# Performance work log

Hardware: AMD Instinct MI355X
Metric: run time of the kernel (lower is better)

## Reference

```python
import jax, jax.numpy as jnp
import numpy as np

ALPHA = 0.2  # leakyrelu negative slope and residual scale


def setup_inputs() -> dict:
    key = jax.random.key(0)
    k1, k2, k3, k4 = jax.random.split(key, 4)
    B, N, C, F = 8, 2048, 128, 128
    text = jax.random.normal(k1, (B, N, C), dtype=jnp.float32)
    adj = jax.random.uniform(k2, (B, N, N), dtype=jnp.float32)  # unused by the layer's math
    W = jax.random.normal(k3, (C, F), dtype=jnp.float32) * (1.0 / np.sqrt(C))
    a = jax.random.normal(k4, (2 * F, 1), dtype=jnp.float32) * 0.1
    return {"text": text, "adj": adj, "W": W, "a": a}


def reference(text, adj, W, a):
    # h: [B, N, F]
    h = jnp.matmul(text, W)
    Fdim = W.shape[1]
    a1 = a[:Fdim, 0]  # applies to source node i
    a2 = a[Fdim:, 0]  # applies to target node j
    e1 = jnp.einsum('bnf,f->bn', h, a1)  # [B, N]
    e2 = jnp.einsum('bnf,f->bn', h, a2)  # [B, N]
    # scores[b,i,j] = leakyrelu(a1.h_i + a2.h_j)  (same as concat-matmul in original)
    scores = jax.nn.leaky_relu(e1[:, :, None] + e2[:, None, :], negative_slope=ALPHA)
    attention = jax.nn.softmax(scores, axis=2)  # [B, N, N]; dropout off (eval)
    h_prime = jnp.matmul(attention, h)  # [B, N, F]
    return jax.nn.elu(h_prime + ALPHA * h)
```

## Files before the change

kernel.cpp:

```cpp
#include <hip/hip_runtime.h>
#include <hip/hip_bf16.h>

#define BB 8
#define NN 2048
#define CC 128
#define FF 128
#define ALPHA 0.2f
#define ROWS 16
#define WTPAD 136
#define CHN 256
#define CLEN 8
#define CSH 3

typedef __hip_bfloat16 bf16;
typedef __attribute__((ext_vector_type(8))) short short8;
typedef __attribute__((ext_vector_type(4))) float f32x4;

__device__ __forceinline__ float ld1(const void* p, int i, int f32) {
    if (f32) return ((const float*)p)[i];
    return __bfloat162float(((const bf16*)p)[i]);
}
__device__ __forceinline__ float2 ld2(const void* p, int pair, int f32) {
    if (f32) return ((const float2*)p)[pair];
    __hip_bfloat162 v = ((const __hip_bfloat162*)p)[pair];
    return make_float2(__bfloat162float(v.x), __bfloat162float(v.y));
}

__global__ __launch_bounds__(256) void k_prep(const void* __restrict__ text,
                                              const void* __restrict__ W,
                                              const void* __restrict__ a,
                                              int* __restrict__ flag,
                                              float* __restrict__ wa1,
                                              float* __restrict__ wa2,
                                              ushort* __restrict__ WT) {
    __shared__ int cnt;
    __shared__ float aL[2 * FF];
    const int t = threadIdx.x;
    if (t == 0) cnt = 0;
    __syncthreads();
    const ushort2* p = (const ushort2*)text;
    int local = 0;
    for (int i = t; i < 1024; i += 256) {
        ushort2 v = p[i];
        float f = __uint_as_float(((unsigned)v.x) << 16);
        if (!(fabsf(f) <= 100.f)) local++;
    }
    atomicAdd(&cnt, local);
    __syncthreads();
    const int f32 = (cnt >= 64) ? 1 : 0;

    if (blockIdx.x == 0) {
        if (t == 0) flag[0] = f32;
        aL[t] = ld1(a, t, f32);
        __syncthreads();
        if (t < CC) {
            float s1 = 0.f, s2 = 0.f;
            for (int f = 0; f < FF; f += 4) {
                float w0 = ld1(W, t * FF + f, f32);
                float w1 = ld1(W, t * FF + f + 1, f32);
                float w2 = ld1(W, t * FF + f + 2, f32);
                float w3 = ld1(W, t * FF + f + 3, f32);
                s1 += w0 * aL[f] + w1 * aL[f + 1] + w2 * aL[f + 2] + w3 * aL[f + 3];
                s2 += w0 * aL[FF + f] + w1 * aL[FF + f + 1] + w2 * aL[FF + f + 2] + w3 * aL[FF + f + 3];
            }
            wa1[t] = s1; wa2[t] = s2;
        }
    } else {
        const int base = (blockIdx.x - 1) * 2048;
        for (int i = 0; i < 8; ++i) {
            int idx = base + i * 256 + t;
            int cc = idx >> 7, f = idx & 127;
            float v = ld1(W, idx, f32);
            bf16 b = __float2bfloat16(v);
            WT[f * CC + cc] = *(const ushort*)&b;
        }
    }
}

__global__ __launch_bounds__(256) void k_e(const void* __restrict__ text,
                                           const float* __restrict__ wa1,
                                           const float* __restrict__ wa2,
                                           float* __restrict__ e1,
                                           float* __restrict__ e2,
                                           unsigned* __restrict__ ukey,
                                           const int* __restrict__ flag) {
    const int f32 = *flag;
    const int wave = threadIdx.x >> 6;
    const int lane = threadIdx.x & 63;
    const int row = blockIdx.x * 4 + wave;
    float2 tv = ld2(text, row * (CC / 2) + lane, f32);
    float s1 = tv.x * wa1[2 * lane] + tv.y * wa1[2 * lane + 1];
    float s2 = tv.x * wa2[2 * lane] + tv.y * wa2[2 * lane + 1];
#pragma unroll
    for (int off = 32; off > 0; off >>= 1) {
        s1 += __shfl_down(s1, off, 64);
        s2 += __shfl_down(s2, off, 64);
    }
    if (lane == 0) {
        e1[row] = s1; e2[row] = s2;
        unsigned m = __float_as_uint(s2);
        m = (m & 0x80000000u) ? ~m : (m | 0x80000000u);
        ukey[row] = (m & 0xFFFFF800u) | (unsigned)(row & (NN - 1));
    }
}

__global__ __launch_bounds__(256) void k_rank(const unsigned* __restrict__ ukey,
                                              const float* __restrict__ e1,
                                              const float* __restrict__ e2,
                                              float* __restrict__ e2s,
                                              int* __restrict__ sidx,
                                              int* __restrict__ lor) {
    __shared__ unsigned kL[NN];
    const int b = blockIdx.x >> 5;
    const int seg = blockIdx.x & 31;
    const int t = threadIdx.x;
    {
        const uint4* src = (const uint4*)(ukey + b * NN);
        ((uint4*)kL)[t] = src[t];
        ((uint4*)kL)[256 + t] = src[256 + t];
    }
    __syncthreads();
    const int lane = t & 63;
    const int wv = t >> 6;
    const int rl = wv * 16 + (lane >> 2);
    const int quarter = lane & 3;
    const int r = seg * 64 + rl;
    const unsigned my = kL[r];
    const float ev = e1[b * NN + r];
    unsigned mt = __float_as_uint(-ev);
    mt = (mt & 0x80000000u) ? ~mt : (mt | 0x80000000u);
    const unsigned tk = mt | 0x7FFu;
    int rank = 0, lo = 0;
    const uint4* q4 = (const uint4*)&kL[quarter * 512];
#pragma unroll 4
    for (int j = 0; j < 128; ++j) {
        uint4 q = q4[j];
        rank += (q.x < my) + (q.y < my) + (q.z < my) + (q.w < my);
        lo   += (q.x <= tk) + (q.y <= tk) + (q.z <= tk) + (q.w <= tk);
    }
    rank += __shfl_xor(rank, 1, 64); lo += __shfl_xor(lo, 1, 64);
    rank += __shfl_xor(rank, 2, 64); lo += __shfl_xor(lo, 2, 64);
    if (quarter == 0) {
        e2s[b * NN + rank] = e2[b * NN + r];
        sidx[b * NN + rank] = r;
        lor[b * NN + r] = lo;
    }
}

__global__ __launch_bounds__(1024) void k_scanZ(const float* __restrict__ e2s,
                                                const float* __restrict__ e1,
                                                const int* __restrict__ lor,
                                                float* __restrict__ rig) {
    __shared__ float Z1L[NN + 1];
    __shared__ float Z2L[NN + 1];
    __shared__ float2 wtot[16];
    __shared__ float2 woff[16];
    const int b = blockIdx.x;
    const int t = threadIdx.x;

    float2 vv = *(const float2*)&e2s[b * NN + 2 * t];
    const float v0 = vv.x, v1 = vv.y;
    float x0a = expf(v0), x0b = expf(ALPHA * v0);
    float x1a = expf(v1), x1b = expf(ALPHA * v1);
    float pa = x0a + x1a, pb = x0b + x1b;
    float sa = pa, sb = pb;
    const int lane = t & 63, wid = t >> 6;
#pragma unroll
    for (int off = 1; off < 64; off <<= 1) {
        float ya = __shfl_up(sa, off, 64);
        float yb = __shfl_up(sb, off, 64);
        if (lane >= off) { sa += ya; sb += yb; }
    }
    if (lane == 63) wtot[wid] = make_float2(sa, sb);
    __syncthreads();
    if (t == 0) {
        float ra = 0.f, rb = 0.f;
        for (int w2 = 0; w2 < 16; ++w2) {
            float2 tt = wtot[w2];
            woff[w2] = make_float2(ra, rb);
            ra += tt.x; rb += tt.y;
        }
    }
    __syncthreads();
    float2 o = woff[wid];
    float pre_a = o.x + sa - pa, pre_b = o.y + sb - pb;
    if (t == 0) { Z1L[0] = 0.f; Z2L[0] = 0.f; }
    Z1L[2 * t + 1] = pre_a + x0a;  Z2L[2 * t + 1] = pre_b + x0b;
    Z1L[2 * t + 2] = pre_a + pa;   Z2L[2 * t + 2] = pre_b + pb;
    __syncthreads();

    const float ZN = Z1L[NN];
#pragma unroll
    for (int rr = 0; rr < 2; ++rr) {
        const int r = t + rr * 1024;
        float ev = e1[b * NN + r];
        float w1 = expf(ev), w2 = expf(ALPHA * ev);
        const int lo = lor[b * NN + r];
        float den = w1 * (ZN - Z1L[lo]) + w2 * Z2L[lo];
        den = fmaxf(den, 1e-30f);
        ((float4*)rig)[b * NN + r] = make_float4(__int_as_float(lo), w1, w2, 1.f / den);
    }
}

__global__ __launch_bounds__(128) void k_tot(const void* __restrict__ text,
                                             const float* __restrict__ e2s,
                                             const int* __restrict__ sidx,
                                             float* __restrict__ T1,
                                             float* __restrict__ T2,
                                             const int* __restrict__ flag) {
    const int f32 = *flag;
    const int b = blockIdx.x / CHN, ch = blockIdx.x % CHN;
    const int c = threadIdx.x;
    float r1 = 0.f, r2 = 0.f;
    const int k0 = ch * CLEN;
#pragma unroll
    for (int kk = 0; kk < CLEN; ++kk) {
        int k = k0 + kk;
        float v = e2s[b * NN + k];
        int j = sidx[b * NN + k];
        float x = ld1(text, (b * NN + j) * CC + c, f32);
        r1 += expf(v) * x;
        r2 += expf(ALPHA * v) * x;
    }
    T1[(b * (CHN + 1) + ch) * CC + c] = r1;
    T2[(b * (CHN + 1) + ch) * CC + c] = r2;
}

__global__ __launch_bounds__(256) void k_scan2(float* __restrict__ T1,
                                               float* __restrict__ T2) {
    __shared__ float2 wt[4];
    const int b = blockIdx.x >> 7, c = blockIdx.x & 127;
    const int ch = threadIdx.x;
    float* P1 = T1 + (size_t)(b * (CHN + 1)) * CC + c;
    float* P2 = T2 + (size_t)(b * (CHN + 1)) * CC + c;
    const float t1 = P1[ch * CC];
    const float t2 = P2[ch * CC];
    float s1 = t1, s2 = t2;
    const int lane = ch & 63, wid = ch >> 6;
#pragma unroll
    for (int off = 1; off < 64; off <<= 1) {
        float y1 = __shfl_up(s1, off, 64);
        float y2 = __shfl_up(s2, off, 64);
        if (lane >= off) { s1 += y1; s2 += y2; }
    }
    if (lane == 63) wt[wid] = make_float2(s1, s2);
    __syncthreads();
    float o1 = 0.f, o2 = 0.f;
#pragma unroll
    for (int w2 = 0; w2 < 4; ++w2)
        if (w2 < wid) { o1 += wt[w2].x; o2 += wt[w2].y; }
    P1[ch * CC] = o1 + s1 - t1;
    P2[ch * CC] = o2 + s2 - t2;
    if (ch == CHN - 1) { P1[CHN * CC] = o1 + s1; P2[CHN * CC] = o2 + s2; }
}

__global__ __launch_bounds__(256) void k_out(const void* __restrict__ text,
                                             const ushort* __restrict__ WT,
                                             const float* __restrict__ T1,
                                             const float* __restrict__ T2,
                                             const float* __restrict__ e2s,
                                             const int* __restrict__ sidx,
                                             const float* __restrict__ rig,
                                             void* __restrict__ out,
                                             const int* __restrict__ flag) {
    __shared__ ushort WTl[FF * WTPAD];
    __shared__ ushort ul[ROWS * WTPAD];
    __shared__ float4 ri[ROWS];
    const int f32 = *flag;
    const int t = threadIdx.x;
    const int b = blockIdx.x / (NN / ROWS);
    const int r0 = (blockIdx.x % (NN / ROWS)) * ROWS;

    {
        const uint4* src = (const uint4*)WT;
#pragma unroll
        for (int i = 0; i < 8; ++i) {
            int idx = i * 256 + t;
            uint4 v = src[idx];
            int f = idx >> 4, cb = idx & 15;
            *(uint4*)&WTl[f * WTPAD + cb * 8] = v;
        }
    }
    if (t < ROWS) ri[t] = ((const float4*)rig)[b * NN + r0 + t];
    __syncthreads();

    {
        const int c = t & 127;
        const int g = t >> 7;
        const float* CB1 = T1 + (size_t)(b * (CHN + 1)) * CC + c;
        const float* CB2 = T2 + (size_t)(b * (CHN + 1)) * CC + c;
        const float* e2sb = e2s + b * NN;
        const int* sxb = sidx + b * NN;
        const float S1 = CB1[CHN * CC];
#pragma unroll
        for (int q = 0; q < 8; ++q) {
            const int rr = g * 8 + q;
            float4 info = ri[rr];
            const int k = __builtin_amdgcn_readfirstlane(__float_as_int(info.x));
            const int c0 = k >> CSH;
            float P1 = CB1[c0 * CC];
            float P2 = CB2[c0 * CC];
            const int j0 = c0 * CLEN;
            const int cnt = k - j0;
            if (cnt > 0) {
                float vv[CLEN - 1]; int jj[CLEN - 1];
#pragma unroll
                for (int i = 0; i < CLEN - 1; ++i) {
                    vv[i] = e2sb[j0 + i];
                    jj[i] = sxb[j0 + i];
                }
#pragma unroll
                for (int i = 0; i < CLEN - 1; ++i) {
                    if (i < cnt) {
                        float x = ld1(text, (b * NN + jj[i]) * CC + c, f32);
                        P1 += expf(vv[i]) * x;
                        P2 += expf(ALPHA * vv[i]) * x;
                    }
                }
            }
            float tc = ld1(text, (b * NN + r0 + rr) * CC + c, f32);
            float u = (info.y * (S1 - P1) + info.z * P2) * info.w + ALPHA * tc;
            bf16 ub = __float2bfloat16(u);
            ul[rr * WTPAD + c] = *(const ushort*)&ub;
        }
    }
    __syncthreads();

    {
        const int wv = t >> 6;
        const int lane = t & 63;
        const int m = lane & 15;
        const int quad = lane >> 4;
        f32x4 acc0 = {0.f, 0.f, 0.f, 0.f};
        f32x4 acc1 = {0.f, 0.f, 0.f, 0.f};
        const int f0 = (wv * 2 + 0) * 16 + m;
        const int f1 = (wv * 2 + 1) * 16 + m;
#pragma unroll
        for (int kt = 0; kt < 4; ++kt) {
            const int ko = kt * 32 + quad * 8;
            short8 afrag = *(const short8*)&ul[m * WTPAD + ko];
            short8 bf0 = *(const short8*)&WTl[f0 * WTPAD + ko];
            short8 bf1 = *(const short8*)&WTl[f1 * WTPAD + ko];
            acc0 = __builtin_amdgcn_mfma_f32_16x16x32_bf16(afrag, bf0, acc0, 0, 0, 0);
            acc1 = __builtin_amdgcn_mfma_f32_16x16x32_bf16(afrag, bf1, acc1, 0, 0, 0);
        }
#pragma unroll
        for (int ft = 0; ft < 2; ++ft) {
            f32x4 acc = ft ? acc1 : acc0;
            const int f = (wv * 2 + ft) * 16 + m;
#pragma unroll
            for (int reg = 0; reg < 4; ++reg) {
                const int urow = quad * 4 + reg;
                float x = acc[reg];
                float y = x > 0.f ? x : expm1f(x);
                const int orow = b * NN + r0 + urow;
                if (f32) ((float*)out)[orow * FF + f] = y;
                else     ((bf16*)out)[orow * FF + f] = __float2bfloat16(y);
            }
        }
    }
}

extern "C" void kernel_launch(void* const* d_in, const int* in_sizes, int n_in,
                              void* d_out, int out_size, void* d_ws, size_t ws_size,
                              hipStream_t stream) {
    const void* text = d_in[0];
    const void* Wp   = (n_in >= 4) ? d_in[2] : d_in[1];
    const void* ap   = (n_in >= 4) ? d_in[3] : d_in[2];
    for (int i = 0; i < n_in; ++i) {
        int s = in_sizes[i];
        if (s == BB * NN * CC)      text = d_in[i];
        else if (s == CC * FF)      Wp = d_in[i];
        else if (s == 2 * FF)       ap = d_in[i];
    }

    float* w = (float*)d_ws;
    size_t off = 0;
    int*      flagp = (int*)(w + off);      off += 16;
    float*    wa1   = w + off;              off += 128;
    float*    wa2   = w + off;              off += 128;
    ushort*   WT    = (ushort*)(w + off);   off += 8192;
    float*    e1    = w + off;              off += BB * NN;
    float*    e2    = w + off;              off += BB * NN;
    unsigned* ukey  = (unsigned*)(w + off); off += BB * NN;
    float*    e2s   = w + off;              off += BB * NN;
    int*      sidx  = (int*)(w + off);      off += BB * NN;
    int*      lor   = (int*)(w + off);      off += BB * NN;
    float*    rig   = w + off;              off += (size_t)4 * BB * NN;
    float*    T1    = w + off;              off += (size_t)BB * (CHN + 1) * CC;
    float*    T2    = w + off;              off += (size_t)BB * (CHN + 1) * CC;

    k_prep<<<9, 256, 0, stream>>>(text, Wp, ap, flagp, wa1, wa2, WT);
    k_e<<<BB * NN / 4, 256, 0, stream>>>(text, wa1, wa2, e1, e2, ukey, flagp);
    k_rank<<<BB * 32, 256, 0, stream>>>(ukey, e1, e2, e2s, sidx, lor);
    k_scanZ<<<BB, 1024, 0, stream>>>(e2s, e1, lor, rig);
    k_tot<<<BB * CHN, 128, 0, stream>>>(text, e2s, sidx, T1, T2, flagp);
    k_scan2<<<BB * CC, 256, 0, stream>>>(T1, T2);
    k_out<<<BB * NN / ROWS, 256, 0, stream>>>(text, WT, T1, T2, e2s, sidx,
                                              rig, d_out, flagp);
}
```

Before: 238.7 us.

## Fuse prep into e-projection kernel and merge Z-scan with chunk totals

Merges the prep kernel (dtype probe, W·a projection, W transpose) into the e1/e2 projection kernel. Each 1024-thread block now recomputes wa1/wa2 locally and uses float4 loads. Also merges the per-batch Z prefix scan and the chunk-total kernel into one launch, using different block ranges. The dtype flag is recomputed in every block instead of being read from workspace, which cuts two launches and a dependency. The cost is redundant W·a work and extra probe reads in every block, and the scan now runs with only 8 blocks of 256 threads.

```diff
diff --git a/kernel.cpp b/kernel.cpp
--- a/kernel.cpp
+++ b/kernel.cpp
@@ -20,87 +20,95 @@
     if (f32) return ((const float*)p)[i];
     return __bfloat162float(((const bf16*)p)[i]);
 }
-__device__ __forceinline__ float2 ld2(const void* p, int pair, int f32) {
-    if (f32) return ((const float2*)p)[pair];
-    __hip_bfloat162 v = ((const __hip_bfloat162*)p)[pair];
-    return make_float2(__bfloat162float(v.x), __bfloat162float(v.y));
-}
-
-__global__ __launch_bounds__(256) void k_prep(const void* __restrict__ text,
-                                              const void* __restrict__ W,
-                                              const void* __restrict__ a,
-                                              int* __restrict__ flag,
-                                              float* __restrict__ wa1,
-                                              float* __restrict__ wa2,
-                                              ushort* __restrict__ WT) {
-    __shared__ int cnt;
-    __shared__ float aL[2 * FF];
-    const int t = threadIdx.x;
-    if (t == 0) cnt = 0;
+
+template <int THREADS>
+__device__ __forceinline__ int probe_f32(const void* text, int* cntLds, int t) {
+    if (t == 0) *cntLds = 0;
     __syncthreads();
     const ushort2* p = (const ushort2*)text;
     int local = 0;
-    for (int i = t; i < 1024; i += 256) {
+    for (int i = t; i < 1024; i += THREADS) {
         ushort2 v = p[i];
         float f = __uint_as_float(((unsigned)v.x) << 16);
         if (!(fabsf(f) <= 100.f)) local++;
     }
-    atomicAdd(&cnt, local);
-    __syncthreads();
-    const int f32 = (cnt >= 64) ? 1 : 0;
-
-    if (blockIdx.x == 0) {
-        if (t == 0) flag[0] = f32;
-        aL[t] = ld1(a, t, f32);
-        __syncthreads();
-        if (t < CC) {
-            float s1 = 0.f, s2 = 0.f;
-            for (int f = 0; f < FF; f += 4) {
-                float w0 = ld1(W, t * FF + f, f32);
-                float w1 = ld1(W, t * FF + f + 1, f32);
-                float w2 = ld1(W, t * FF + f + 2, f32);
-                float w3 = ld1(W, t * FF + f + 3, f32);
-                s1 += w0 * aL[f] + w1 * aL[f + 1] + w2 * aL[f + 2] + w3 * aL[f + 3];
-                s2 += w0 * aL[FF + f] + w1 * aL[FF + f + 1] + w2 * aL[FF + f + 2] + w3 * aL[FF + f + 3];
-            }
-            wa1[t] = s1; wa2[t] = s2;
-        }
-    } else {
-        const int base = (blockIdx.x - 1) * 2048;
-        for (int i = 0; i < 8; ++i) {
-            int idx = base + i * 256 + t;
+    atomicAdd(cntLds, local);
+    __syncthreads();
+    return (*cntLds >= 64) ? 1 : 0;
+}
+
+__global__ __launch_bounds__(1024) void k_ew(const void* __restrict__ text,
+                                             const void* __restrict__ W,
+                                             const void* __restrict__ a,
+                                             float* __restrict__ e1,
+                                             float* __restrict__ e2,
+                                             unsigned* __restrict__ ukey,
+                                             ushort* __restrict__ WT) {
+    __shared__ int cnt;
+    __shared__ float aL[2 * FF];
+    __shared__ float wa1L[CC], wa2L[CC];
+    const int t = threadIdx.x;
+    const int f32 = probe_f32<1024>(text, &cnt, t);
+
+    if (blockIdx.x >= 512) {
+        const int base = (blockIdx.x - 512) * 2048;
+#pragma unroll
+        for (int i = 0; i < 2; ++i) {
+            int idx = base + i * 1024 + t;
             int cc = idx >> 7, f = idx & 127;
             float v = ld1(W, idx, f32);
             bf16 b = __float2bfloat16(v);
             WT[f * CC + cc] = *(const ushort*)&b;
         }
-    }
-}
-
-__global__ __launch_bounds__(256) void k_e(const void* __restrict__ text,
-                                           const float* __restrict__ wa1,
-                                           const float* __restrict__ wa2,
-                                           float* __restrict__ e1,
-                                           float* __restrict__ e2,
-                                           unsigned* __restrict__ ukey,
-                                           const int* __restrict__ flag) {
-    const int f32 = *flag;
-    const int wave = threadIdx.x >> 6;
-    const int lane = threadIdx.x & 63;
-    const int row = blockIdx.x * 4 + wave;
-    float2 tv = ld2(text, row * (CC / 2) + lane, f32);
-    float s1 = tv.x * wa1[2 * lane] + tv.y * wa1[2 * lane + 1];
-    float s2 = tv.x * wa2[2 * lane] + tv.y * wa2[2 * lane + 1];
-#pragma unroll
-    for (int off = 32; off > 0; off >>= 1) {
-        s1 += __shfl_down(s1, off, 64);
-        s2 += __shfl_down(s2, off, 64);
-    }
-    if (lane == 0) {
-        e1[row] = s1; e2[row] = s2;
+        return;
+    }
+
+    if (t < 2 * FF) aL[t] = ld1(a, t, f32);
+    __syncthreads();
+    if (t < CC) {
+        float s1 = 0.f, s2 = 0.f;
+        for (int f = 0; f < FF; f += 4) {
+            float w0 = ld1(W, t * FF + f, f32);
+            float w1 = ld1(W, t * FF + f + 1, f32);
+            float w2 = ld1(W, t * FF + f + 2, f32);
+            float w3 = ld1(W, t * FF + f + 3, f32);
+            s1 += w0 * aL[f] + w1 * aL[f + 1] + w2 * aL[f + 2] + w3 * aL[f + 3];
+            s2 += w0 * aL[FF + f] + w1 * aL[FF + f + 1] + w2 * aL[FF + f + 2] + w3 * aL[FF + f + 3];
+        }
+        wa1L[t] = s1; wa2L[t] = s2;
+    }
+    __syncthreads();
+
+    const int wv = t >> 6;
+    const int lane = t & 63;
+    const int h = lane >> 5;
+    const int l = lane & 31;
+    const int r = blockIdx.x * 32 + wv * 2 + h;
+    const int c0 = 4 * l;
+    float s1, s2;
+    if (f32) {
+        float4 q = ((const float4*)text)[r * 32 + l];
+        s1 = q.x * wa1L[c0] + q.y * wa1L[c0 + 1] + q.z * wa1L[c0 + 2] + q.w * wa1L[c0 + 3];
+        s2 = q.x * wa2L[c0] + q.y * wa2L[c0 + 1] + q.z * wa2L[c0 + 2] + q.w * wa2L[c0 + 3];
+    } else {
+        uint2 q = ((const uint2*)text)[r * 32 + l];
+        float v0 = __uint_as_float((q.x & 0xFFFFu) << 16);
+        float v1 = __uint_as_float(q.x & 0xFFFF0000u);
+        float v2 = __uint_as_float((q.y & 0xFFFFu) << 16);
+        float v3 = __uint_as_float(q.y & 0xFFFF0000u);
+        s1 = v0 * wa1L[c0] + v1 * wa1L[c0 + 1] + v2 * wa1L[c0 + 2] + v3 * wa1L[c0 + 3];
+        s2 = v0 * wa2L[c0] + v1 * wa2L[c0 + 1] + v2 * wa2L[c0 + 2] + v3 * wa2L[c0 + 3];
+    }
+#pragma unroll
+    for (int m = 1; m <= 16; m <<= 1) {
+        s1 += __shfl_xor(s1, m, 64);
+        s2 += __shfl_xor(s2, m, 64);
+    }
+    if (l == 0) {
+        e1[r] = s1; e2[r] = s2;
         unsigned m = __float_as_uint(s2);
         m = (m & 0x80000000u) ? ~m : (m | 0x80000000u);
-        ukey[row] = (m & 0xFFFFF800u) | (unsigned)(row & (NN - 1));
+        ukey[r] = (m & 0xFFFFF800u) | (unsigned)(r & (NN - 1));
     }
 }
 
@@ -147,22 +155,51 @@
     }
 }
 
-__global__ __launch_bounds__(1024) void k_scanZ(const float* __restrict__ e2s,
-                                                const float* __restrict__ e1,
-                                                const int* __restrict__ lor,
-                                                float* __restrict__ rig) {
+__global__ __launch_bounds__(256) void k_totZ(const void* __restrict__ text,
+                                              const float* __restrict__ e2s,
+                                              const int* __restrict__ sidx,
+                                              const float* __restrict__ e1,
+                                              const int* __restrict__ lor,
+                                              float* __restrict__ T1,
+                                              float* __restrict__ T2,
+                                              float* __restrict__ rig) {
+    __shared__ int cnt;
     __shared__ float Z1L[NN + 1];
     __shared__ float Z2L[NN + 1];
-    __shared__ float2 wtot[16];
-    __shared__ float2 woff[16];
-    const int b = blockIdx.x;
+    __shared__ float2 wtL[4];
     const int t = threadIdx.x;
 
-    float2 vv = *(const float2*)&e2s[b * NN + 2 * t];
-    const float v0 = vv.x, v1 = vv.y;
-    float x0a = expf(v0), x0b = expf(ALPHA * v0);
-    float x1a = expf(v1), x1b = expf(ALPHA * v1);
-    float pa = x0a + x1a, pb = x0b + x1b;
+    if (blockIdx.x < 1024) {
+        const int f32 = probe_f32<256>(text, &cnt, t);
+        const int gch = blockIdx.x * 2 + (t >> 7);
+        const int b = gch >> 8, ch = gch & (CHN - 1);
+        const int c = t & 127;
+        float r1 = 0.f, r2 = 0.f;
+        const int k0 = ch * CLEN;
+#pragma unroll
+        for (int kk = 0; kk < CLEN; ++kk) {
+            int k = k0 + kk;
+            float v = e2s[b * NN + k];
+            int j = sidx[b * NN + k];
+            float x = ld1(text, (b * NN + j) * CC + c, f32);
+            r1 += expf(v) * x;
+            r2 += expf(ALPHA * v) * x;
+        }
+        T1[(b * (CHN + 1) + ch) * CC + c] = r1;
+        T2[(b * (CHN + 1) + ch) * CC + c] = r2;
+        return;
+    }
+
+    const int b = blockIdx.x - 1024;
+    float xa[8], xb[8], ca[8], cb[8];
+    float pa = 0.f, pb = 0.f;
+#pragma unroll
+    for (int i = 0; i < 8; ++i) {
+        float v = e2s[b * NN + 8 * t + i];
+        xa[i] = expf(v); xb[i] = expf(ALPHA * v);
+        pa += xa[i]; ca[i] = pa;
+        pb += xb[i]; cb[i] = pb;
+    }
     float sa = pa, sb = pb;
     const int lane = t & 63, wid = t >> 6;
 #pragma unroll
@@ -171,28 +208,24 @@
         float yb = __shfl_up(sb, off, 64);
         if (lane >= off) { sa += ya; sb += yb; }
     }
-    if (lane == 63) wtot[wid] = make_float2(sa, sb);
-    __syncthreads();
-    if (t == 0) {
-        float ra = 0.f, rb = 0.f;
-        for (int w2 = 0; w2 < 16; ++w2) {
-            float2 tt = wtot[w2];
-            woff[w2] = make_float2(ra, rb);
-            ra += tt.x; rb += tt.y;
-        }
-    }
-    __syncthreads();
-    float2 o = woff[wid];
-    float pre_a = o.x + sa - pa, pre_b = o.y + sb - pb;
+    if (lane == 63) wtL[wid] = make_float2(sa, sb);
+    __syncthreads();
+    float oa = 0.f, ob = 0.f;
+#pragma unroll
+    for (int w2 = 0; w2 < 4; ++w2)
+        if (w2 < wid) { oa += wtL[w2].x; ob += wtL[w2].y; }
+    const float base_a = oa + sa - pa, base_b = ob + sb - pb;
     if (t == 0) { Z1L[0] = 0.f; Z2L[0] = 0.f; }
-    Z1L[2 * t + 1] = pre_a + x0a;  Z2L[2 * t + 1] = pre_b + x0b;
-    Z1L[2 * t + 2] = pre_a + pa;   Z2L[2 * t + 2] = pre_b + pb;
-    __syncthreads();
-
+#pragma unroll
+    for (int i = 0; i < 8; ++i) {
+        Z1L[8 * t + 1 + i] = base_a + ca[i];
+        Z2L[8 * t + 1 + i] = base_b + cb[i];
+    }
+    __syncthreads();
     const float ZN = Z1L[NN];
 #pragma unroll
-    for (int rr = 0; rr < 2; ++rr) {
-        const int r = t + rr * 1024;
+    for (int i = 0; i < 8; ++i) {
+        const int r = 8 * t + i;
         float ev = e1[b * NN + r];
         float w1 = expf(ev), w2 = expf(ALPHA * ev);
         const int lo = lor[b * NN + r];
@@ -200,30 +233,6 @@
         den = fmaxf(den, 1e-30f);
         ((float4*)rig)[b * NN + r] = make_float4(__int_as_float(lo), w1, w2, 1.f / den);
     }
-}
-
-__global__ __launch_bounds__(128) void k_tot(const void* __restrict__ text,
-                                             const float* __restrict__ e2s,
-                                             const int* __restrict__ sidx,
-                                             float* __restrict__ T1,
-                                             float* __restrict__ T2,
-                                             const int* __restrict__ flag) {
-    const int f32 = *flag;
-    const int b = blockIdx.x / CHN, ch = blockIdx.x % CHN;
-    const int c = threadIdx.x;
-    float r1 = 0.f, r2 = 0.f;
-    const int k0 = ch * CLEN;
-#pragma unroll
-    for (int kk = 0; kk < CLEN; ++kk) {
-        int k = k0 + kk;
-        float v = e2s[b * NN + k];
-        int j = sidx[b * NN + k];
-        float x = ld1(text, (b * NN + j) * CC + c, f32);
-        r1 += expf(v) * x;
-        r2 += expf(ALPHA * v) * x;
-    }
-    T1[(b * (CHN + 1) + ch) * CC + c] = r1;
-    T2[(b * (CHN + 1) + ch) * CC + c] = r2;
 }
 
 __global__ __launch_bounds__(256) void k_scan2(float* __restrict__ T1,
@@ -261,13 +270,13 @@
                                              const float* __restrict__ e2s,
                                              const int* __restrict__ sidx,
                                              const float* __restrict__ rig,
-                                             void* __restrict__ out,
-                                             const int* __restrict__ flag) {
+                                             void* __restrict__ out) {
+    __shared__ int cnt;
     __shared__ ushort WTl[FF * WTPAD];
     __shared__ ushort ul[ROWS * WTPAD];
     __shared__ float4 ri[ROWS];
-    const int f32 = *flag;
     const int t = threadIdx.x;
+    const int f32 = probe_f32<256>(text, &cnt, t);
     const int b = blockIdx.x / (NN / ROWS);
     const int r0 = (blockIdx.x % (NN / ROWS)) * ROWS;
 
@@ -301,8 +310,8 @@
             float P1 = CB1[c0 * CC];
             float P2 = CB2[c0 * CC];
             const int j0 = c0 * CLEN;
-            const int cnt = k - j0;
-            if (cnt > 0) {
+            const int rcnt = k - j0;
+            if (rcnt > 0) {
                 float vv[CLEN - 1]; int jj[CLEN - 1];
 #pragma unroll
                 for (int i = 0; i < CLEN - 1; ++i) {
@@ -311,7 +320,7 @@
                 }
 #pragma unroll
                 for (int i = 0; i < CLEN - 1; ++i) {
-                    if (i < cnt) {
+                    if (i < rcnt) {
                         float x = ld1(text, (b * NN + jj[i]) * CC + c, f32);
                         P1 += expf(vv[i]) * x;
                         P2 += expf(ALPHA * vv[i]) * x;
@@ -376,9 +385,6 @@
 
     float* w = (float*)d_ws;
     size_t off = 0;
-    int*      flagp = (int*)(w + off);      off += 16;
-    float*    wa1   = w + off;              off += 128;
-    float*    wa2   = w + off;              off += 128;
     ushort*   WT    = (ushort*)(w + off);   off += 8192;
     float*    e1    = w + off;              off += BB * NN;
     float*    e2    = w + off;              off += BB * NN;
@@ -390,12 +396,10 @@
     float*    T1    = w + off;              off += (size_t)BB * (CHN + 1) * CC;
     float*    T2    = w + off;              off += (size_t)BB * (CHN + 1) * CC;
 
-    k_prep<<<9, 256, 0, stream>>>(text, Wp, ap, flagp, wa1, wa2, WT);
-    k_e<<<BB * NN / 4, 256, 0, stream>>>(text, wa1, wa2, e1, e2, ukey, flagp);
+    k_ew<<<520, 1024, 0, stream>>>(text, Wp, ap, e1, e2, ukey, WT);
     k_rank<<<BB * 32, 256, 0, stream>>>(ukey, e1, e2, e2s, sidx, lor);
-    k_scanZ<<<BB, 1024, 0, stream>>>(e2s, e1, lor, rig);
-    k_tot<<<BB * CHN, 128, 0, stream>>>(text, e2s, sidx, T1, T2, flagp);
+    k_totZ<<<1032, 256, 0, stream>>>(text, e2s, sidx, e1, lor, T1, T2, rig);
     k_scan2<<<BB * CC, 256, 0, stream>>>(T1, T2);
     k_out<<<BB * NN / ROWS, 256, 0, stream>>>(text, WT, T1, T2, e2s, sidx,
-                                              rig, d_out, flagp);
-}
+                                              rig, d_out);
+}
```

New measurement: 245.7 us. 1.03x slower.
